# Kernel tuning notes

Measured on AMD Instinct MI355X. Metric: run time of the kernel, lower is better.

Reference implementation:

```python
import jax, jax.numpy as jnp
import numpy as np

H = 2048          # hidden_size
I = 768           # moe_intermediate_size
E = 64            # num_experts
TOP_K = 8         # num_experts_per_tok (norm_topk_prob=True)
B, S = 1, 1024


def setup_inputs() -> dict:
    key = jax.random.key(0)
    ks = jax.random.split(key, 5)
    scale = 0.02
    return {
        "hidden_states": jax.random.normal(ks[0], (B, S, H), dtype=jnp.float32),
        "W_router": jax.random.normal(ks[1], (H, E), dtype=jnp.float32) * scale,
        "W_gate": jax.random.normal(ks[2], (E, H, I), dtype=jnp.float32) * scale,
        "W_up": jax.random.normal(ks[3], (E, H, I), dtype=jnp.float32) * scale,
        "W_down": jax.random.normal(ks[4], (E, I, H), dtype=jnp.float32) * scale,
    }


def reference(hidden_states, W_router, W_gate, W_up, W_down):
    b, s, h = hidden_states.shape
    x = hidden_states.reshape(-1, h)                      # [T, H]

    # --- Qwen3MoeTopKRouter: linear gate -> fp32 softmax -> top-k -> renorm ---
    logits = x @ W_router                                 # [T, E]
    probs = jax.nn.softmax(logits.astype(jnp.float32), axis=-1)
    top_w, top_idx = jax.lax.top_k(probs, TOP_K)          # [T, K]
    top_w = top_w / jnp.sum(top_w, axis=-1, keepdims=True)  # norm_topk_prob
    top_w = top_w.astype(x.dtype)

    # combine weights per (token, expert): zero if expert not selected
    comb = jnp.sum(jax.nn.one_hot(top_idx, E, dtype=x.dtype) * top_w[..., None], axis=1)  # [T, E]

    # --- per-expert SwiGLU MLP: down(silu(gate(x)) * up(x)), dense-masked ---
    g = jnp.einsum('th,ehi->eti', x, W_gate)              # [E, T, I]
    u = jnp.einsum('th,ehi->eti', x, W_up)                # [E, T, I]
    hmid = jax.nn.silu(g) * u                             # [E, T, I]
    # fold combine weight into the intermediate to avoid an [E, T, H] buffer
    hmid = hmid * comb.T[:, :, None]                      # [E, T, I]
    out = jnp.einsum('eti,eih->th', hmid, W_down)         # [T, H]

    return out.reshape(b, s, h)
```

## Files before the change

### kernel.cpp

```cpp
#include <hip/hip_runtime.h>
#include <hip/hip_bf16.h>

#define H_DIM 2048
#define I_DIM 768
#define NEXP 64
#define TOPK 8
#define NTOK 1024
#define BM 256
#define BKS 32

typedef float f32x4 __attribute__((ext_vector_type(4)));
typedef unsigned int u32x4 __attribute__((ext_vector_type(4)));
typedef unsigned int u32x2 __attribute__((ext_vector_type(2)));
typedef short bf16v8 __attribute__((ext_vector_type(8)));
typedef unsigned short u16x8 __attribute__((ext_vector_type(8)));
typedef unsigned int u32;

#define NTLOAD __builtin_nontemporal_load

#define WS_NEEDED 50954752ull

__device__ inline unsigned short f2bf(float f) {
    union { float f; u32 u; } v; v.f = f;
    u32 r = (v.u + 0x7FFFu + ((v.u >> 16) & 1u)) >> 16;
    return (unsigned short)r;
}
__device__ inline u32 pack2(float a, float b) {
    return (u32)f2bf(a) | ((u32)f2bf(b) << 16);
}

__global__ void zero_kernel(float4* p, int n4) {
    int i = blockIdx.x * blockDim.x + threadIdx.x;
    if (i < n4) p[i] = (float4){0.f, 0.f, 0.f, 0.f};
}

__global__ void xconv_kernel(const float4* __restrict__ x, ushort4* __restrict__ xbf, int n4) {
    int i = blockIdx.x * blockDim.x + threadIdx.x;
    if (i < n4) {
        float4 v = x[i];
        ushort4 o;
        o.x = f2bf(v.x); o.y = f2bf(v.y); o.z = f2bf(v.z); o.w = f2bf(v.w);
        xbf[i] = o;
    }
}

__global__ __launch_bounds__(256) void router_kernel(
    const float* __restrict__ x, const float* __restrict__ Wr,
    int* __restrict__ topk_idx, float* __restrict__ topk_w)
{
    const int t   = blockIdx.x;
    const int tid = threadIdx.x;
    const int lane = tid & 63;
    const int wv   = tid >> 6;
    __shared__ float xs[H_DIM];
    __shared__ float red[4][64];

    const float* xrow = x + (size_t)t * H_DIM;
    {
        const float4* src = (const float4*)xrow;
        float4* dst = (float4*)xs;
        dst[tid]       = src[tid];
        dst[tid + 256] = src[tid + 256];
    }
    __syncthreads();

    float acc = 0.f;
    const int h0 = wv * 512;
    #pragma unroll 8
    for (int h = h0; h < h0 + 512; ++h) acc += xs[h] * Wr[(size_t)h * NEXP + lane];
    red[wv][lane] = acc;
    __syncthreads();

    if (tid < 64) {
        const int e = tid;
        float logit = red[0][e] + red[1][e] + red[2][e] + red[3][e];

        float m = logit;
        #pragma unroll
        for (int o = 32; o > 0; o >>= 1) m = fmaxf(m, __shfl_xor(m, o));
        float p = __expf(logit - m);
        float s = p;
        #pragma unroll
        for (int o = 32; o > 0; o >>= 1) s += __shfl_xor(s, o);
        float prob = p / s;

        float myp = prob;
        float kw[TOPK]; int kid[TOPK]; float wsum = 0.f;
        #pragma unroll
        for (int k = 0; k < TOPK; ++k) {
            float v = myp; int bi = e;
            #pragma unroll
            for (int o = 32; o > 0; o >>= 1) {
                float ov = __shfl_xor(v, o);
                int   oi = __shfl_xor(bi, o);
                if (ov > v || (ov == v && oi < bi)) { v = ov; bi = oi; }
            }
            kw[k] = v; kid[k] = bi; wsum += v;
            if (e == bi) myp = -1.f;
        }
        if (e == 0) {
            float inv = 1.f / wsum;
            #pragma unroll
            for (int k = 0; k < TOPK; ++k) {
                topk_idx[t * TOPK + k] = kid[k];
                topk_w[t * TOPK + k]   = kw[k] * inv;
            }
        }
    }
}

__global__ __launch_bounds__(64) void listbuild_kernel(
    const int* __restrict__ topk_idx, const float* __restrict__ topk_w,
    int* __restrict__ counts, int* __restrict__ lists, float* __restrict__ wlist,
    int* __restrict__ invmap)
{
    const int e = blockIdx.x;
    const int lane = threadIdx.x;
    int n = 0;
    for (int base = 0; base < NTOK * TOPK; base += 64) {
        int s = base + lane;
        int idx = topk_idx[s];
        bool match = (idx == e);
        unsigned long long mask = __ballot(match);
        int pre = __popcll(mask & ((1ull << lane) - 1ull));
        if (match) {
            lists[e * NTOK + n + pre] = s >> 3;
            wlist[e * NTOK + n + pre] = topk_w[s];
            invmap[s] = n + pre;
        }
        n += __popcll(mask);
    }
    if (lane == 0) counts[e] = n;
}

__global__ __launch_bounds__(64) void scan_kernel(
    const int* __restrict__ counts, int* __restrict__ offsets)
{
    int e = threadIdx.x;
    int v = counts[e];
    int xacc = v;
    #pragma unroll
    for (int o = 1; o < 64; o <<= 1) {
        int y = __shfl_up(xacc, o);
        if (e >= o) xacc += y;
    }
    offsets[e] = xacc - v;
}

#define MFMA_BF16 __builtin_amdgcn_mfma_f32_16x16x32_bf16

__global__ __launch_bounds__(512) void gateup_kernel(
    const unsigned short* __restrict__ xbf,
    const float* __restrict__ Wg, const float* __restrict__ Wu,
    const int* __restrict__ counts, const int* __restrict__ offsets,
    const int* __restrict__ lists, const float* __restrict__ wlist,
    unsigned short* __restrict__ hmid)
{
    const int b  = blockIdx.x;
    const int wg = (b & 7) * 192 + (b >> 3);
    const int itile = wg % 24;
    const int e     = wg / 24;

    const int count = counts[e];
    if (count == 0) return;
    const int off = offsets[e];
    const int i0 = itile * 32;

    __shared__ unsigned short Alds[BM][40];
    __shared__ u32 Bgl[32 * 20];
    __shared__ u32 Bul[32 * 20];

    const int tid  = threadIdx.x;
    const int lane = tid & 63;
    const int wid  = tid >> 6;
    const int wm   = wid >> 1, wn = wid & 1;
    const int kb   = lane >> 4;
    const int l15  = lane & 15;

    const int ar = tid >> 1;
    const int ah = (tid & 1) * 16;
    const int bnn  = tid & 31;
    const int bkq  = (tid >> 5) & 7;
    const int bmat = tid >> 8;
    const float* WB = (bmat ? Wu : Wg) + (size_t)e * H_DIM * I_DIM + i0 + bnn;
    const int key4w = 4 * ((bnn >> 3) & 3);
    u32* bdst = (bmat ? Bul : Bgl) + bnn * 20 + ((2 * bkq) ^ key4w);
    const int brn   = wn * 16 + l15;
    const int key4r = 4 * ((brn >> 3) & 3);

    for (int mstart = 0; mstart < count; mstart += BM) {
        const int pr = mstart + ar;
        const bool aact = pr < count;
        const unsigned short* xrow = xbf + (size_t)(aact ? lists[e * NTOK + pr] : 0) * H_DIM + ah;
        const bool mact = (mstart + wm * 64) < count;

        f32x4 accg[4], accu[4];
        #pragma unroll
        for (int i = 0; i < 4; ++i) {
            accg[i] = (f32x4){0.f, 0.f, 0.f, 0.f};
            accu[i] = (f32x4){0.f, 0.f, 0.f, 0.f};
        }

        u32x4 aA0, aA1, aB0, aB1, aC0, aC1, aD0, aD1;
        float bA0, bA1, bA2, bA3;
        float bB0, bB1, bB2, bB3;
        float bC0, bC1, bC2, bC3;
        float bD0, bD1, bD2, bD3;

#define GU_LOADA(P0,P1,h)                                                       \
        if (aact) {                                                             \
            const u32x4* pa_ = (const u32x4*)(xrow + (h));                      \
            P0 = pa_[0]; P1 = pa_[1];                                           \
        }
#define GU_LOADB(R0,R1,R2,R3,h)                                                 \
        {                                                                       \
            R0 = NTLOAD(WB + (size_t)((h) + 4 * bkq)     * I_DIM);              \
            R1 = NTLOAD(WB + (size_t)((h) + 4 * bkq + 1) * I_DIM);              \
            R2 = NTLOAD(WB + (size_t)((h) + 4 * bkq + 2) * I_DIM);              \
            R3 = NTLOAD(WB + (size_t)((h) + 4 * bkq + 3) * I_DIM);              \
        }
#define GU_STOREA(P0,P1)                                                        \
        if (aact) {                                                             \
            *(u32x4*)&Alds[ar][ah]     = P0;                                    \
            *(u32x4*)&Alds[ar][ah + 8] = P1;                                    \
        }
#define GU_STOREB(R0,R1,R2,R3)                                                  \
        {                                                                       \
            u32x2 w_; w_.x = pack2(R0, R1); w_.y = pack2(R2, R3);               \
            *(u32x2*)bdst = w_;                                                 \
        }
#define GU_MFMA()                                                               \
        if (mact) {                                                             \
            bf16v8 af[4], bg, bu;                                               \
            _Pragma("unroll")                                                   \
            for (int mf = 0; mf < 4; ++mf)                                      \
                af[mf] = *(const bf16v8*)&Alds[wm * 64 + mf * 16 + l15][kb * 8];\
            bg = *(const bf16v8*)&Bgl[brn * 20 + ((4 * kb) ^ key4r)];           \
            bu = *(const bf16v8*)&Bul[brn * 20 + ((4 * kb) ^ key4r)];           \
            _Pragma("unroll")                                                   \
            for (int mf = 0; mf < 4; ++mf) {                                    \
                accg[mf] = MFMA_BF16(af[mf], bg, accg[mf], 0, 0, 0);            \
                accu[mf] = MFMA_BF16(af[mf], bu, accu[mf], 0, 0, 0);            \
            }                                                                   \
        }
#define GU_PHASE(P0,P1,R0,R1,R2,R3,nh)                                          \
        GU_STOREA(P0, P1); GU_STOREB(R0, R1, R2, R3);                           \
        __syncthreads();                                                        \
        if ((nh) < H_DIM) { GU_LOADB(R0, R1, R2, R3, (nh)); GU_LOADA(P0, P1, (nh)); } \
        GU_MFMA();                                                              \
        __syncthreads();

        GU_LOADB(bA0, bA1, bA2, bA3, 0);        GU_LOADA(aA0, aA1, 0);
        GU_LOADB(bB0, bB1, bB2, bB3, BKS);      GU_LOADA(aB0, aB1, BKS);
        GU_LOADB(bC0, bC1, bC2, bC3, 2 * BKS);  GU_LOADA(aC0, aC1, 2 * BKS);
        GU_LOADB(bD0, bD1, bD2, bD3, 3 * BKS);  GU_LOADA(aD0, aD1, 3 * BKS);

        for (int hh = 0; hh < H_DIM; hh += 4 * BKS) {
            GU_PHASE(aA0, aA1, bA0, bA1, bA2, bA3, hh + 4 * BKS);
            GU_PHASE(aB0, aB1, bB0, bB1, bB2, bB3, hh + 5 * BKS);
            GU_PHASE(aC0, aC1, bC0, bC1, bC2, bC3, hh + 6 * BKS);
            GU_PHASE(aD0, aD1, bD0, bD1, bD2, bD3, hh + 7 * BKS);
        }
#undef GU_LOADA
#undef GU_LOADB
#undef GU_STOREA
#undef GU_STOREB
#undef GU_MFMA
#undef GU_PHASE

        if (mact) {
            #pragma unroll
            for (int mf = 0; mf < 4; ++mf)
                #pragma unroll
                for (int r = 0; r < 4; ++r) {
                    int pos = mstart + wm * 64 + mf * 16 + kb * 4 + r;
                    if (pos < count) {
                        float wgt = wlist[e * NTOK + pos];
                        float g = accg[mf][r], u = accu[mf][r];
                        float s = 1.f / (1.f + __expf(-g));
                        hmid[(size_t)(off + pos) * I_DIM + i0 + wn * 16 + l15] = f2bf(g * s * u * wgt);
                    }
                }
        }
    }
}

template <bool USE_PART>
__global__ __launch_bounds__(512) void down_kernel(
    const unsigned short* __restrict__ hmid, const float* __restrict__ Wd,
    const int* __restrict__ counts, const int* __restrict__ offsets,
    const int* __restrict__ lists, float* __restrict__ out,
    unsigned short* __restrict__ part)
{
    const int b  = blockIdx.x;
    const int wg = (b & 7) * 512 + (b >> 3);
    const int htile = wg % 64;
    const int e     = wg / 64;

    const int count = counts[e];
    if (count == 0) return;
    const int off = offsets[e];
    const int h0 = htile * 32;

    __shared__ unsigned short Alds[BM][40];
    __shared__ u32 Bdl[32 * 20];

    const int tid  = threadIdx.x;
    const int lane = tid & 63;
    const int wid  = tid >> 6;
    const int wm   = wid >> 1, wn = wid & 1;
    const int kb   = lane >> 4;
    const int l15  = lane & 15;

    const int ar = tid >> 1;
    const int ah = (tid & 1) * 16;
    const int bnn  = tid & 31;
    const int bkq  = (tid >> 5) & 7;
    const bool bact = tid < 256;
    const float* WB = Wd + (size_t)e * I_DIM * H_DIM + h0 + bnn;
    const int key4w = 4 * ((bnn >> 3) & 3);
    u32* bdst = Bdl + bnn * 20 + ((2 * bkq) ^ key4w);
    const int brn   = wn * 16 + l15;
    const int key4r = 4 * ((brn >> 3) & 3);

    for (int mstart = 0; mstart < count; mstart += BM) {
        const int pr = mstart + ar;
        const bool aact = pr < count;
        const unsigned short* hrow = hmid + (size_t)(off + (aact ? pr : 0)) * I_DIM + ah;
        const bool mact = (mstart + wm * 64) < count;

        f32x4 acc[4];
        #pragma unroll
        for (int i = 0; i < 4; ++i) acc[i] = (f32x4){0.f, 0.f, 0.f, 0.f};

        u32x4 aA0, aA1, aB0, aB1, aC0, aC1, aD0, aD1;
        float bA0, bA1, bA2, bA3;
        float bB0, bB1, bB2, bB3;
        float bC0, bC1, bC2, bC3;
        float bD0, bD1, bD2, bD3;

#define DN_LOADA(P0,P1,k)                                                       \
        if (aact) {                                                             \
            const u32x4* p_ = (const u32x4*)(hrow + (k));                       \
            P0 = p_[0]; P1 = p_[1];                                             \
        }
#define DN_LOADB(R0,R1,R2,R3,k)                                                 \
        if (bact) {                                                             \
            R0 = NTLOAD(WB + (size_t)((k) + 4 * bkq)     * H_DIM);              \
            R1 = NTLOAD(WB + (size_t)((k) + 4 * bkq + 1) * H_DIM);              \
            R2 = NTLOAD(WB + (size_t)((k) + 4 * bkq + 2) * H_DIM);              \
            R3 = NTLOAD(WB + (size_t)((k) + 4 * bkq + 3) * H_DIM);              \
        }
#define DN_STOREA(P0,P1)                                                        \
        if (aact) {                                                             \
            *(u32x4*)&Alds[ar][ah]     = P0;                                    \
            *(u32x4*)&Alds[ar][ah + 8] = P1;                                    \
        }
#define DN_STOREB(R0,R1,R2,R3)                                                  \
        if (bact) {                                                             \
            u32x2 w_; w_.x = pack2(R0, R1); w_.y = pack2(R2, R3);               \
            *(u32x2*)bdst = w_;                                                 \
        }
#define DN_MFMA()                                                               \
        if (mact) {                                                             \
            bf16v8 af[4], bd;                                                   \
            _Pragma("unroll")                                                   \
            for (int mf = 0; mf < 4; ++mf)                                      \
                af[mf] = *(const bf16v8*)&Alds[wm * 64 + mf * 16 + l15][kb * 8];\
            bd = *(const bf16v8*)&Bdl[brn * 20 + ((4 * kb) ^ key4r)];           \
            _Pragma("unroll")                                                   \
            for (int mf = 0; mf < 4; ++mf)                                      \
                acc[mf] = MFMA_BF16(af[mf], bd, acc[mf], 0, 0, 0);              \
        }
#define DN_PHASE(P0,P1,R0,R1,R2,R3,nk)                                          \
        DN_STOREA(P0, P1); DN_STOREB(R0, R1, R2, R3);                           \
        __syncthreads();                                                        \
        if ((nk) < I_DIM) { DN_LOADB(R0, R1, R2, R3, (nk)); DN_LOADA(P0, P1, (nk)); } \
        DN_MFMA();                                                              \
        __syncthreads();

        DN_LOADB(bA0, bA1, bA2, bA3, 0);        DN_LOADA(aA0, aA1, 0);
        DN_LOADB(bB0, bB1, bB2, bB3, BKS);      DN_LOADA(aB0, aB1, BKS);
        DN_LOADB(bC0, bC1, bC2, bC3, 2 * BKS);  DN_LOADA(aC0, aC1, 2 * BKS);
        DN_LOADB(bD0, bD1, bD2, bD3, 3 * BKS);  DN_LOADA(aD0, aD1, 3 * BKS);

        for (int ii = 0; ii < I_DIM; ii += 4 * BKS) {
            DN_PHASE(aA0, aA1, bA0, bA1, bA2, bA3, ii + 4 * BKS);
            DN_PHASE(aB0, aB1, bB0, bB1, bB2, bB3, ii + 5 * BKS);
            DN_PHASE(aC0, aC1, bC0, bC1, bC2, bC3, ii + 6 * BKS);
            DN_PHASE(aD0, aD1, bD0, bD1, bD2, bD3, ii + 7 * BKS);
        }
#undef DN_LOADA
#undef DN_LOADB
#undef DN_STOREA
#undef DN_STOREB
#undef DN_MFMA
#undef DN_PHASE

        if (mact) {
            #pragma unroll
            for (int mf = 0; mf < 4; ++mf)
                #pragma unroll
                for (int r = 0; r < 4; ++r) {
                    int pos = mstart + wm * 64 + mf * 16 + kb * 4 + r;
                    if (pos < count) {
                        if constexpr (USE_PART) {
                            part[(size_t)(off + pos) * H_DIM + h0 + wn * 16 + l15] =
                                f2bf(acc[mf][r]);
                        } else {
                            int tok = lists[e * NTOK + pos];
                            atomicAdd(&out[(size_t)tok * H_DIM + h0 + wn * 16 + l15],
                                      acc[mf][r]);
                        }
                    }
                }
        }
    }
}

__global__ __launch_bounds__(256) void reduce_kernel(
    const unsigned short* __restrict__ part,
    const int* __restrict__ topk_idx, const int* __restrict__ invmap,
    const int* __restrict__ offsets, float* __restrict__ out)
{
    const int t   = blockIdx.x;
    const int tid = threadIdx.x;
    __shared__ int slots[TOPK];
    if (tid < TOPK) {
        int s = t * TOPK + tid;
        slots[tid] = offsets[topk_idx[s]] + invmap[s];
    }
    __syncthreads();

    const int c = tid * 8;
    float acc[8] = {0.f, 0.f, 0.f, 0.f, 0.f, 0.f, 0.f, 0.f};
    #pragma unroll
    for (int k = 0; k < TOPK; ++k) {
        u16x8 v = *(const u16x8*)&part[(size_t)slots[k] * H_DIM + c];
        #pragma unroll
        for (int j = 0; j < 8; ++j)
            acc[j] += __uint_as_float((u32)(unsigned short)v[j] << 16);
    }
    float4* dst = (float4*)&out[(size_t)t * H_DIM + c];
    dst[0] = (float4){acc[0], acc[1], acc[2], acc[3]};
    dst[1] = (float4){acc[4], acc[5], acc[6], acc[7]};
}

extern "C" void kernel_launch(void* const* d_in, const int* in_sizes, int n_in,
                              void* d_out, int out_size, void* d_ws, size_t ws_size,
                              hipStream_t stream) {
    const float* x  = (const float*)d_in[0];
    const float* Wr = (const float*)d_in[1];
    const float* Wg = (const float*)d_in[2];
    const float* Wu = (const float*)d_in[3];
    const float* Wd = (const float*)d_in[4];
    float* out = (float*)d_out;

    char* ws = (char*)d_ws;
    int*   topk_idx = (int*)  (ws + 0);
    float* topk_w   = (float*)(ws + 32768);
    int*   counts   = (int*)  (ws + 65536);
    int*   offsets  = (int*)  (ws + 65792);
    int*   lists    = (int*)  (ws + 66048);
    float* wlist    = (float*)(ws + 328192);
    int*   invmap   = (int*)  (ws + 590336);
    unsigned short* hmid = (unsigned short*)(ws + 623104);
    unsigned short* xbf  = (unsigned short*)(ws + 13206016);
    unsigned short* part = (unsigned short*)(ws + 17400320);

    const bool usePart = ws_size >= WS_NEEDED;

    hipLaunchKernelGGL(xconv_kernel, dim3((NTOK * H_DIM / 4 + 255) / 256), dim3(256), 0, stream,
                       (const float4*)x, (ushort4*)xbf, NTOK * H_DIM / 4);
    hipLaunchKernelGGL(router_kernel, dim3(NTOK), dim3(256), 0, stream,
                       x, Wr, topk_idx, topk_w);
    hipLaunchKernelGGL(listbuild_kernel, dim3(NEXP), dim3(64), 0, stream,
                       topk_idx, topk_w, counts, lists, wlist, invmap);
    hipLaunchKernelGGL(scan_kernel, dim3(1), dim3(64), 0, stream,
                       counts, offsets);
    hipLaunchKernelGGL(gateup_kernel, dim3(24 * NEXP), dim3(512), 0, stream,
                       xbf, Wg, Wu, counts, offsets, lists, wlist, hmid);
    if (usePart) {
        hipLaunchKernelGGL((down_kernel<true>), dim3(64 * NEXP), dim3(512), 0, stream,
                           hmid, Wd, counts, offsets, lists, out, part);
        hipLaunchKernelGGL(reduce_kernel, dim3(NTOK), dim3(256), 0, stream,
                           part, topk_idx, invmap, offsets, out);
    } else {
        const int nout4 = NTOK * H_DIM / 4;
        hipLaunchKernelGGL(zero_kernel, dim3((nout4 + 255) / 256), dim3(256), 0, stream,
                           (float4*)out, nout4);
        hipLaunchKernelGGL((down_kernel<false>), dim3(64 * NEXP), dim3(512), 0, stream,
                           hmid, Wd, counts, offsets, lists, out, part);
    }
}
```

Measured before the change: 533.2 us.

## Double-buffer LDS tiles with one barrier per phase in MoE GEMMs

Both the gate/up and down expert GEMM kernels now use two LDS buffers, so each k-step needs one raw barrier (after an lgkmcnt wait) instead of two __syncthreads. The register prefetch depth drops from four stages to two to offset the extra LDS and register pressure. MFMA sections are wrapped in s_setprio to favour math waves. This cuts barrier stalls but shortens global-load latency hiding and doubles LDS use, which may lower occupancy.

```diff
diff --git a/kernel.cpp b/kernel.cpp
--- a/kernel.cpp
+++ b/kernel.cpp
@@ -148,6 +148,8 @@
 }
 
 #define MFMA_BF16 __builtin_amdgcn_mfma_f32_16x16x32_bf16
+#define LGKM0()  asm volatile("s_waitcnt lgkmcnt(0)" ::: "memory")
+#define RAWBAR() __builtin_amdgcn_s_barrier()
 
 __global__ __launch_bounds__(512) void gateup_kernel(
     const unsigned short* __restrict__ xbf,
@@ -166,9 +168,9 @@
     const int off = offsets[e];
     const int i0 = itile * 32;
 
-    __shared__ unsigned short Alds[BM][40];
-    __shared__ u32 Bgl[32 * 20];
-    __shared__ u32 Bul[32 * 20];
+    __shared__ unsigned short Alds[2][BM][40];
+    __shared__ u32 Bgl[2][32 * 20];
+    __shared__ u32 Bul[2][32 * 20];
 
     const int tid  = threadIdx.x;
     const int lane = tid & 63;
@@ -184,7 +186,7 @@
     const int bmat = tid >> 8;
     const float* WB = (bmat ? Wu : Wg) + (size_t)e * H_DIM * I_DIM + i0 + bnn;
     const int key4w = 4 * ((bnn >> 3) & 3);
-    u32* bdst = (bmat ? Bul : Bgl) + bnn * 20 + ((2 * bkq) ^ key4w);
+    const int bwoff = bnn * 20 + ((2 * bkq) ^ key4w);
     const int brn   = wn * 16 + l15;
     const int key4r = 4 * ((brn >> 3) & 3);
 
@@ -201,11 +203,9 @@
             accu[i] = (f32x4){0.f, 0.f, 0.f, 0.f};
         }
 
-        u32x4 aA0, aA1, aB0, aB1, aC0, aC1, aD0, aD1;
+        u32x4 aA0, aA1, aB0, aB1;
         float bA0, bA1, bA2, bA3;
         float bB0, bB1, bB2, bB3;
-        float bC0, bC1, bC2, bC3;
-        float bD0, bD1, bD2, bD3;
 
 #define GU_LOADA(P0,P1,h)                                                       \
         if (aact) {                                                             \
@@ -219,52 +219,49 @@
             R2 = NTLOAD(WB + (size_t)((h) + 4 * bkq + 2) * I_DIM);              \
             R3 = NTLOAD(WB + (size_t)((h) + 4 * bkq + 3) * I_DIM);              \
         }
-#define GU_STOREA(P0,P1)                                                        \
+#define GU_STORE(BUF,P0,P1,R0,R1,R2,R3)                                         \
         if (aact) {                                                             \
-            *(u32x4*)&Alds[ar][ah]     = P0;                                    \
-            *(u32x4*)&Alds[ar][ah + 8] = P1;                                    \
-        }
-#define GU_STOREB(R0,R1,R2,R3)                                                  \
+            *(u32x4*)&Alds[BUF][ar][ah]     = P0;                               \
+            *(u32x4*)&Alds[BUF][ar][ah + 8] = P1;                               \
+        }                                                                       \
         {                                                                       \
             u32x2 w_; w_.x = pack2(R0, R1); w_.y = pack2(R2, R3);               \
-            *(u32x2*)bdst = w_;                                                 \
-        }
-#define GU_MFMA()                                                               \
+            *(u32x2*)((bmat ? Bul[BUF] : Bgl[BUF]) + bwoff) = w_;               \
+        }
+#define GU_MFMA(BUF)                                                            \
         if (mact) {                                                             \
             bf16v8 af[4], bg, bu;                                               \
             _Pragma("unroll")                                                   \
             for (int mf = 0; mf < 4; ++mf)                                      \
-                af[mf] = *(const bf16v8*)&Alds[wm * 64 + mf * 16 + l15][kb * 8];\
-            bg = *(const bf16v8*)&Bgl[brn * 20 + ((4 * kb) ^ key4r)];           \
-            bu = *(const bf16v8*)&Bul[brn * 20 + ((4 * kb) ^ key4r)];           \
+                af[mf] = *(const bf16v8*)&Alds[BUF][wm * 64 + mf * 16 + l15][kb * 8]; \
+            bg = *(const bf16v8*)&Bgl[BUF][brn * 20 + ((4 * kb) ^ key4r)];      \
+            bu = *(const bf16v8*)&Bul[BUF][brn * 20 + ((4 * kb) ^ key4r)];      \
             _Pragma("unroll")                                                   \
             for (int mf = 0; mf < 4; ++mf) {                                    \
                 accg[mf] = MFMA_BF16(af[mf], bg, accg[mf], 0, 0, 0);            \
                 accu[mf] = MFMA_BF16(af[mf], bu, accu[mf], 0, 0, 0);            \
             }                                                                   \
         }
-#define GU_PHASE(P0,P1,R0,R1,R2,R3,nh)                                          \
-        GU_STOREA(P0, P1); GU_STOREB(R0, R1, R2, R3);                           \
-        __syncthreads();                                                        \
+#define GU_PHASE(BUF,P0,P1,R0,R1,R2,R3,nh)                                      \
+        GU_STORE(BUF, P0, P1, R0, R1, R2, R3);                                  \
         if ((nh) < H_DIM) { GU_LOADB(R0, R1, R2, R3, (nh)); GU_LOADA(P0, P1, (nh)); } \
-        GU_MFMA();                                                              \
+        LGKM0();                                                                \
+        RAWBAR();                                                               \
+        __builtin_amdgcn_s_setprio(1);                                          \
+        GU_MFMA(BUF);                                                           \
+        __builtin_amdgcn_s_setprio(0);
+
+        GU_LOADB(bA0, bA1, bA2, bA3, 0);    GU_LOADA(aA0, aA1, 0);
+        GU_LOADB(bB0, bB1, bB2, bB3, BKS);  GU_LOADA(aB0, aB1, BKS);
+
+        for (int hh = 0; hh < H_DIM; hh += 2 * BKS) {
+            GU_PHASE(0, aA0, aA1, bA0, bA1, bA2, bA3, hh + 2 * BKS);
+            GU_PHASE(1, aB0, aB1, bB0, bB1, bB2, bB3, hh + 3 * BKS);
+        }
         __syncthreads();
-
-        GU_LOADB(bA0, bA1, bA2, bA3, 0);        GU_LOADA(aA0, aA1, 0);
-        GU_LOADB(bB0, bB1, bB2, bB3, BKS);      GU_LOADA(aB0, aB1, BKS);
-        GU_LOADB(bC0, bC1, bC2, bC3, 2 * BKS);  GU_LOADA(aC0, aC1, 2 * BKS);
-        GU_LOADB(bD0, bD1, bD2, bD3, 3 * BKS);  GU_LOADA(aD0, aD1, 3 * BKS);
-
-        for (int hh = 0; hh < H_DIM; hh += 4 * BKS) {
-            GU_PHASE(aA0, aA1, bA0, bA1, bA2, bA3, hh + 4 * BKS);
-            GU_PHASE(aB0, aB1, bB0, bB1, bB2, bB3, hh + 5 * BKS);
-            GU_PHASE(aC0, aC1, bC0, bC1, bC2, bC3, hh + 6 * BKS);
-            GU_PHASE(aD0, aD1, bD0, bD1, bD2, bD3, hh + 7 * BKS);
-        }
 #undef GU_LOADA
 #undef GU_LOADB
-#undef GU_STOREA
-#undef GU_STOREB
+#undef GU_STORE
 #undef GU_MFMA
 #undef GU_PHASE
 
@@ -302,8 +299,8 @@
     const int off = offsets[e];
     const int h0 = htile * 32;
 
-    __shared__ unsigned short Alds[BM][40];
-    __shared__ u32 Bdl[32 * 20];
+    __shared__ unsigned short Alds[2][BM][40];
+    __shared__ u32 Bdl[2][32 * 20];
 
     const int tid  = threadIdx.x;
     const int lane = tid & 63;
@@ -319,7 +316,7 @@
     const bool bact = tid < 256;
     const float* WB = Wd + (size_t)e * I_DIM * H_DIM + h0 + bnn;
     const int key4w = 4 * ((bnn >> 3) & 3);
-    u32* bdst = Bdl + bnn * 20 + ((2 * bkq) ^ key4w);
+    const int bwoff = bnn * 20 + ((2 * bkq) ^ key4w);
     const int brn   = wn * 16 + l15;
     const int key4r = 4 * ((brn >> 3) & 3);
 
@@ -333,11 +330,9 @@
         #pragma unroll
         for (int i = 0; i < 4; ++i) acc[i] = (f32x4){0.f, 0.f, 0.f, 0.f};
 
-        u32x4 aA0, aA1, aB0, aB1, aC0, aC1, aD0, aD1;
+        u32x4 aA0, aA1, aB0, aB1;
         float bA0, bA1, bA2, bA3;
         float bB0, bB1, bB2, bB3;
-        float bC0, bC1, bC2, bC3;
-        float bD0, bD1, bD2, bD3;
 
 #define DN_LOADA(P0,P1,k)                                                       \
         if (aact) {                                                             \
@@ -351,49 +346,46 @@
             R2 = NTLOAD(WB + (size_t)((k) + 4 * bkq + 2) * H_DIM);              \
             R3 = NTLOAD(WB + (size_t)((k) + 4 * bkq + 3) * H_DIM);              \
         }
-#define DN_STOREA(P0,P1)                                                        \
+#define DN_STORE(BUF,P0,P1,R0,R1,R2,R3)                                         \
         if (aact) {                                                             \
-            *(u32x4*)&Alds[ar][ah]     = P0;                                    \
-            *(u32x4*)&Alds[ar][ah + 8] = P1;                                    \
-        }
-#define DN_STOREB(R0,R1,R2,R3)                                                  \
+            *(u32x4*)&Alds[BUF][ar][ah]     = P0;                               \
+            *(u32x4*)&Alds[BUF][ar][ah + 8] = P1;                               \
+        }                                                                       \
         if (bact) {                                                             \
             u32x2 w_; w_.x = pack2(R0, R1); w_.y = pack2(R2, R3);               \
-            *(u32x2*)bdst = w_;                                                 \
-        }
-#define DN_MFMA()                                                               \
+            *(u32x2*)(Bdl[BUF] + bwoff) = w_;                                   \
+        }
+#define DN_MFMA(BUF)                                                            \
         if (mact) {                                                             \
             bf16v8 af[4], bd;                                                   \
             _Pragma("unroll")                                                   \
             for (int mf = 0; mf < 4; ++mf)                                      \
-                af[mf] = *(const bf16v8*)&Alds[wm * 64 + mf * 16 + l15][kb * 8];\
-            bd = *(const bf16v8*)&Bdl[brn * 20 + ((4 * kb) ^ key4r)];           \
+                af[mf] = *(const bf16v8*)&Alds[BUF][wm * 64 + mf * 16 + l15][kb * 8]; \
+            bd = *(const bf16v8*)&Bdl[BUF][brn * 20 + ((4 * kb) ^ key4r)];      \
             _Pragma("unroll")                                                   \
             for (int mf = 0; mf < 4; ++mf)                                      \
                 acc[mf] = MFMA_BF16(af[mf], bd, acc[mf], 0, 0, 0);              \
         }
-#define DN_PHASE(P0,P1,R0,R1,R2,R3,nk)                                          \
-        DN_STOREA(P0, P1); DN_STOREB(R0, R1, R2, R3);                           \
-        __syncthreads();                                                        \
+#define DN_PHASE(BUF,P0,P1,R0,R1,R2,R3,nk)                                      \
+        DN_STORE(BUF, P0, P1, R0, R1, R2, R3);                                  \
         if ((nk) < I_DIM) { DN_LOADB(R0, R1, R2, R3, (nk)); DN_LOADA(P0, P1, (nk)); } \
-        DN_MFMA();                                                              \
+        LGKM0();                                                                \
+        RAWBAR();                                                               \
+        __builtin_amdgcn_s_setprio(1);                                          \
+        DN_MFMA(BUF);                                                           \
+        __builtin_amdgcn_s_setprio(0);
+
+        DN_LOADB(bA0, bA1, bA2, bA3, 0);    DN_LOADA(aA0, aA1, 0);
+        DN_LOADB(bB0, bB1, bB2, bB3, BKS);  DN_LOADA(aB0, aB1, BKS);
+
+        for (int ii = 0; ii < I_DIM; ii += 2 * BKS) {
+            DN_PHASE(0, aA0, aA1, bA0, bA1, bA2, bA3, ii + 2 * BKS);
+            DN_PHASE(1, aB0, aB1, bB0, bB1, bB2, bB3, ii + 3 * BKS);
+        }
         __syncthreads();
-
-        DN_LOADB(bA0, bA1, bA2, bA3, 0);        DN_LOADA(aA0, aA1, 0);
-        DN_LOADB(bB0, bB1, bB2, bB3, BKS);      DN_LOADA(aB0, aB1, BKS);
-        DN_LOADB(bC0, bC1, bC2, bC3, 2 * BKS);  DN_LOADA(aC0, aC1, 2 * BKS);
-        DN_LOADB(bD0, bD1, bD2, bD3, 3 * BKS);  DN_LOADA(aD0, aD1, 3 * BKS);
-
-        for (int ii = 0; ii < I_DIM; ii += 4 * BKS) {
-            DN_PHASE(aA0, aA1, bA0, bA1, bA2, bA3, ii + 4 * BKS);
-            DN_PHASE(aB0, aB1, bB0, bB1, bB2, bB3, ii + 5 * BKS);
-            DN_PHASE(aC0, aC1, bC0, bC1, bC2, bC3, ii + 6 * BKS);
-            DN_PHASE(aD0, aD1, bD0, bD1, bD2, bD3, ii + 7 * BKS);
-        }
 #undef DN_LOADA
 #undef DN_LOADB
-#undef DN_STOREA
-#undef DN_STOREB
+#undef DN_STORE
 #undef DN_MFMA
 #undef DN_PHASE
 
```

Result: faster. 476.4 us (-10.7%).
